# Optimization experiments

Measured on AMD Instinct MI355X. Metric: run time of the kernel, lower is better.

The kernel has to match this reference:

```python
import jax, jax.numpy as jnp
import numpy as np
import math

B, L, D = 2, 2048, 256
N_SETS, PLANES_PER_SET = 4, 4
TOTAL_PLANES = N_SETS * PLANES_PER_SET  # 16
POS_PLANES = 16
LTM_PLANES = POS_PLANES
PI = math.pi
LN_EPS = 1e-5


def _mlp2(x, w1, b1, w2, b2):
    h = jax.nn.gelu(x @ w1 + b1, approximate=False)  # torch nn.GELU default = erf
    return h @ w2 + b2


def setup_inputs() -> dict:
    key = jax.random.key(0)
    ks = iter(jax.random.split(key, 40))
    def W(shape):
        return jax.random.normal(next(ks), shape, jnp.float32) / np.float32(np.sqrt(shape[0]))
    z = lambda *s: jnp.zeros(s, jnp.float32)
    return dict(
        x=jax.random.normal(next(ks), (B, L, D), jnp.float32),
        ke_w1=W((D, D)), ke_b1=z(D), ke_w2=W((D, TOTAL_PLANES)), ke_b2=z(TOTAL_PLANES),
        qe_w1=W((D, D)), qe_b1=z(D), qe_w2=W((D, TOTAL_PLANES)), qe_b2=z(TOTAL_PLANES),
        v_w=W((D, D)), v_b=z(D),
        out_ln_g=jnp.ones(D, jnp.float32), out_ln_b=z(D),
        out_w=W((D, D)), out_b=z(D),
        set_weights=jnp.ones(N_SETS, jnp.float32),
        pos_weight=jnp.ones((), jnp.float32),
        gate_w1=W((D, D // 2)), gate_b1=z(D // 2), gate_w2=W((D // 2, 1)), gate_b2=z(1),
        lke_w1=W((D, D)), lke_b1=z(D), lke_w2=W((D, LTM_PLANES)), lke_b2=z(LTM_PLANES),
        surprise_scale=jnp.asarray(5.0, jnp.float32), surprise_bias=jnp.asarray(0.0, jnp.float32),
        resonance_scale=jnp.asarray(5.0, jnp.float32), resonance_threshold=jnp.asarray(0.3, jnp.float32),
        ltm_weight=jnp.asarray(0.5, jnp.float32),
        pos_freqs=jnp.exp(jnp.arange(POS_PLANES, dtype=jnp.float32) * (-math.log(10000.0) / POS_PLANES)),
        ltm_binding_mem=((jax.random.normal(next(ks), (LTM_PLANES, D))
                          + 1j * jax.random.normal(next(ks), (LTM_PLANES, D))) * 0.5).astype(jnp.complex64),
        ltm_count=jnp.asarray(100.0, jnp.float32),
    )


def reference(x, ke_w1, ke_b1, ke_w2, ke_b2, qe_w1, qe_b1, qe_w2, qe_b2,
              v_w, v_b, out_ln_g, out_ln_b, out_w, out_b,
              set_weights, pos_weight, gate_w1, gate_b1, gate_w2, gate_b2,
              lke_w1, lke_b1, lke_w2, lke_b2,
              surprise_scale, surprise_bias, resonance_scale, resonance_threshold,
              ltm_weight, pos_freqs, ltm_binding_mem, ltm_count):
    B_, L_, D_ = x.shape
    key_phasor = jnp.exp(1j * (jnp.tanh(_mlp2(x, ke_w1, ke_b1, ke_w2, ke_b2)) * PI))    # (B,L,16) complex64
    query_phasor = jnp.exp(1j * (jnp.tanh(_mlp2(x, qe_w1, qe_b1, qe_w2, qe_b2)) * PI))  # (B,L,16)
    kp = key_phasor.reshape(B_, L_, N_SETS, PLANES_PER_SET)
    qp = query_phasor.reshape(B_, L_, N_SETS, PLANES_PER_SET)
    weights = jax.nn.softmax(set_weights)
    V_real = x @ v_w + v_b                                                              # (B,L,D)

    # --- cross-bank surprise gate (n_sets > 1 branch) ---
    joint_key = jnp.prod(kp, axis=2)    # (B,L,PP)
    joint_query = jnp.prod(qp, axis=2)
    km = jnp.cumsum(joint_key, axis=1)
    key_memory = jnp.concatenate([jnp.zeros_like(km[:, :1]), km[:, :-1]], axis=1)       # shifted cumsum
    resonance_mag = jnp.abs(key_memory * jnp.conj(joint_query)).mean(-1, keepdims=True)
    positions = jnp.maximum(jnp.arange(L_, dtype=x.dtype), 1.0)
    norm_res = resonance_mag / jnp.sqrt(positions)[None, :, None]
    scale = jnp.clip(resonance_scale, 1.0, 20.0)
    thr = jnp.clip(resonance_threshold, 0.1, 0.9)
    surprise = 0.5 * (1.0 - jnp.tanh(scale * (norm_res - thr)))
    write_gate = jax.nn.sigmoid(surprise_scale * (surprise - 0.5) + surprise_bias)      # (B,L,1)
    Vg = (V_real * write_gate).astype(jnp.complex64)

    # --- cross-bank retrieval over joint (product) phasors ---
    bound = joint_key[..., None] * Vg[:, :, None, :]                                     # (B,L,PP,D)
    mem = jnp.cumsum(bound, axis=1)
    cross = jnp.real((mem * jnp.conj(joint_query)[..., None]).sum(2))                    # (B,L,D)

    # --- per-bank retrieval over all 16 planes ---
    bound_all = key_phasor[..., None] * Vg[:, :, None, :]                                # (B,L,16,D)
    mem_all = jnp.cumsum(bound_all, axis=1)
    ret_all = mem_all * jnp.conj(query_phasor)[..., None]
    per_bank = jnp.real(ret_all.reshape(B_, L_, N_SETS, PLANES_PER_SET, D_).sum(3))      # (B,L,S,D)
    total = (per_bank * weights[None, None, :, None]).sum(2)
    total = (total + cross) / (N_SETS + 1)

    # --- positional phase plane ---
    pos_phase = jnp.arange(L_, dtype=x.dtype)[:, None] * pos_freqs * (2.0 * PI)          # (L,16)
    pos_phasor = jnp.exp(1j * pos_phase)
    Vc = V_real.astype(jnp.complex64)
    bound_pos = pos_phasor[None, :, :, None] * Vc[:, :, None, :]                         # (B,L,16,D)
    mem_pos = jnp.cumsum(bound_pos, axis=1)
    ret_pos = jnp.real((mem_pos * jnp.conj(pos_phasor)[None, :, :, None]).sum(2))        # (B,L,D)
    gate = jax.nn.sigmoid(_mlp2(x, gate_w1, gate_b1, gate_w2, gate_b2))                  # (B,L,1)
    total = gate * total + (1.0 - gate) * (jax.nn.sigmoid(pos_weight) * ret_pos)

    # --- long-term memory retrieval (inference path; buffers are constants) ---
    ltm_phasor = jnp.exp(1j * (jnp.tanh(_mlp2(x, lke_w1, lke_b1, lke_w2, lke_b2)) * PI)) # (B,L,16)
    persistent = jnp.real((ltm_binding_mem[None, None] * jnp.conj(ltm_phasor)[..., None]).sum(2))
    pnorm = jnp.sqrt(jnp.maximum(ltm_count, 1.0) * LTM_PLANES)
    total = total + jax.nn.sigmoid(ltm_weight) * (persistent / pnorm)

    # --- to_out: LayerNorm + Linear ---
    mu = total.mean(-1, keepdims=True)
    var = ((total - mu) ** 2).mean(-1, keepdims=True)
    h = (total - mu) / jnp.sqrt(var + LN_EPS) * out_ln_g + out_ln_b
    return h @ out_w + out_b
```

## Files before the change

kernel.cpp:

```cpp
#include <hip/hip_runtime.h>
#include <hip/hip_bf16.h>
#include <math.h>

#define BB 2
#define LL 2048
#define DD 256
#define NT (BB*LL)
#define HCOLS 896
#define NCOLS 1152
#define KBIG 768
#define FDIM 80
#define CC 64
#define NC (NT/CC)
#define NCB (LL/CC)
#define SST (FDIM*DD)
#define PI_F 3.14159265358979323846f

typedef __attribute__((ext_vector_type(8))) short s8frag;
typedef __attribute__((ext_vector_type(4))) float f4acc;

#define GLDS16(g, l) __builtin_amdgcn_global_load_lds( \
    (const __attribute__((address_space(1))) void*)(g), \
    (__attribute__((address_space(3))) void*)(l), 16, 0, 0)

__device__ __forceinline__ float gelu_erf(float v) {
    return 0.5f * v * (1.0f + erff(v * 0.70710678118654752440f));
}
__device__ __forceinline__ float sigmoidf_(float v) {
    return 1.0f / (1.0f + expf(-v));
}
__device__ __forceinline__ unsigned short bf16bits(__hip_bfloat16 h) {
    return *reinterpret_cast<unsigned short*>(&h);
}

#define K0A_BLKS (NT * DD / 4 / 256)
#define K0B_TW   22
#define K0B_BLKS ((KBIG / 64) * K0B_TW)
#define K0C_BLKS (4 * 16 * 768 / 256)
#define K0D_BLKS 5
__global__ __launch_bounds__(256) void k0_prep(
    const float* __restrict__ x,
    const float* __restrict__ ke_w1, const float* __restrict__ ke_b1,
    const float* __restrict__ qe_w1, const float* __restrict__ qe_b1,
    const float* __restrict__ lke_w1, const float* __restrict__ lke_b1,
    const float* __restrict__ gate_w1, const float* __restrict__ gate_b1,
    const float* __restrict__ v_w, const float* __restrict__ v_b,
    const float* __restrict__ ke_w2, const float* __restrict__ qe_w2,
    const float* __restrict__ lke_w2, const float* __restrict__ gate_w2,
    const float* __restrict__ out_w,
    __hip_bfloat16* __restrict__ xhi, __hip_bfloat16* __restrict__ xlo,
    __hip_bfloat16* __restrict__ BT, float* __restrict__ bcat,
    __hip_bfloat16* __restrict__ W2T, __hip_bfloat16* __restrict__ OWT)
{
    __shared__ float tile[64][65];
    const int b = blockIdx.x, tid = threadIdx.x;
    if (b < K0A_BLKS) {
        int idx = b * 256 + tid;
        float4 v = reinterpret_cast<const float4*>(x)[idx];
        float vv[4] = {v.x, v.y, v.z, v.w};
        #pragma unroll
        for (int j = 0; j < 4; ++j) {
            __hip_bfloat16 h = __float2bfloat16(vv[j]);
            xhi[idx * 4 + j] = h;
            xlo[idx * 4 + j] = __float2bfloat16(vv[j] - __bfloat162float(h));
        }
    } else if (b < K0A_BLKS + K0B_BLKS) {
        int bb = b - K0A_BLKS;
        int bk = bb / K0B_TW, bn = bb - bk * K0B_TW;
        int kp0 = bk * 64, n0 = bn * 64;
        int seg = kp0 >> 8;
        int k0 = kp0 - seg * 256;
        #pragma unroll 4
        for (int i = 0; i < 16; ++i) {
            int kl = i * 4 + (tid >> 6);
            int nl = tid & 63;
            int k = k0 + kl, n = n0 + nl;
            float w;
            if (n < 256)       w = ke_w1[k * 256 + n];
            else if (n < 512)  w = qe_w1[k * 256 + (n - 256)];
            else if (n < 768)  w = lke_w1[k * 256 + (n - 512)];
            else if (n < 896)  w = gate_w1[k * 128 + (n - 768)];
            else if (n < 1152) w = v_w[k * 256 + (n - 896)];
            else               w = out_w[k * 256 + (n - 1152)];
            tile[kl][nl] = w;
        }
        __syncthreads();
        #pragma unroll 4
        for (int i = 0; i < 16; ++i) {
            int nl = i * 4 + (tid >> 6);
            int kpl = tid & 63;
            float w = tile[kpl][nl];
            __hip_bfloat16 hi = __float2bfloat16(w);
            __hip_bfloat16 out = (seg == 1)
                ? __float2bfloat16(w - __bfloat162float(hi)) : hi;
            if (n0 < 1152)
                BT[(size_t)(n0 + nl) * KBIG + kp0 + kpl] = out;
            else
                OWT[(size_t)(n0 + nl - 1152) * KBIG + kp0 + kpl] = out;
        }
    } else if (b < K0A_BLKS + K0B_BLKS + K0C_BLKS) {
        int idx = (b - K0A_BLKS - K0B_BLKS) * 256 + tid;
        int g = idx / (16 * 768);
        int rem = idx - g * (16 * 768);
        int n = rem / 768;
        int kp = rem - n * 768;
        float w = 0.0f;
        int seg;
        if (g < 3) {
            seg = kp >> 8;
            int k = kp & 255;
            const float* W = (g == 0) ? ke_w2 : (g == 1) ? qe_w2 : lke_w2;
            w = W[k * 16 + n];
        } else {
            seg = kp >> 7;
            int k = kp & 127;
            if (n == 0 && kp < 384) w = gate_w2[k];
            else { seg = 0; w = 0.0f; }
        }
        __hip_bfloat16 hi = __float2bfloat16(w);
        __hip_bfloat16 out = (seg == 1) ? __float2bfloat16(w - __bfloat162float(hi)) : hi;
        W2T[idx] = out;
    } else {
        int n = (b - K0A_BLKS - K0B_BLKS - K0C_BLKS) * 256 + tid;
        if (n < NCOLS) {
            float bia;
            if (n < 256)      bia = ke_b1[n];
            else if (n < 512) bia = qe_b1[n - 256];
            else if (n < 768) bia = lke_b1[n - 512];
            else if (n < 896) bia = gate_b1[n - 768];
            else              bia = v_b[n - 896];
            bcat[n] = bia;
        }
    }
}

__global__ __launch_bounds__(256) void k1_mfma(
    const __hip_bfloat16* __restrict__ xhi, const __hip_bfloat16* __restrict__ xlo,
    const __hip_bfloat16* __restrict__ BT, const float* __restrict__ bcat,
    __hip_bfloat16* __restrict__ Hhi, __hip_bfloat16* __restrict__ Hlo,
    float* __restrict__ V)
{
    __shared__ __align__(16) short As[128 * 64];
    __shared__ __align__(16) short Bs[64 * 64];
    const int tid = threadIdx.x;
    const int wave = tid >> 6, lane = tid & 63;
    const int wr = wave >> 1, wc = wave & 1;
    const int bm = blockIdx.x, bn = blockIdx.y;
    const int lg = lane >> 4, lr = lane & 15;

    f4acc acc[4][2] = {};

    for (int kt = 0; kt < KBIG / 64; ++kt) {
        const int k0 = kt * 64;
        const __hip_bfloat16* xsrc = (kt < 8) ? xhi : xlo;
        const int kcol = (kt < 8) ? (k0 & 255) : (k0 - 512);
        #pragma unroll
        for (int j = 0; j < 4; ++j) {
            int r0 = wave * 32 + j * 8;
            int row = r0 + (lane >> 3);
            int ch = (lane & 7) ^ (row & 7);
            GLDS16(xsrc + (size_t)(bm * 128 + row) * DD + kcol + ch * 8, &As[r0 * 64]);
        }
        #pragma unroll
        for (int j = 0; j < 2; ++j) {
            int r0 = wave * 16 + j * 8;
            int row = r0 + (lane >> 3);
            int ch = (lane & 7) ^ (row & 7);
            GLDS16(BT + (size_t)(bn * 64 + row) * KBIG + k0 + ch * 8, &Bs[r0 * 64]);
        }
        __syncthreads();
        #pragma unroll
        for (int kk = 0; kk < 2; ++kk) {
            s8frag a[4], b[2];
            #pragma unroll
            for (int i = 0; i < 4; ++i) {
                int arow = wr * 64 + i * 16 + lr;
                int slot = (kk * 4 + lg) ^ (arow & 7);
                a[i] = *reinterpret_cast<const s8frag*>(&As[arow * 64 + slot * 8]);
            }
            #pragma unroll
            for (int i = 0; i < 2; ++i) {
                int brow = wc * 32 + i * 16 + lr;
                int slot = (kk * 4 + lg) ^ (brow & 7);
                b[i] = *reinterpret_cast<const s8frag*>(&Bs[brow * 64 + slot * 8]);
            }
            #pragma unroll
            for (int mi = 0; mi < 4; ++mi)
                #pragma unroll
                for (int ni = 0; ni < 2; ++ni)
                    acc[mi][ni] = __builtin_amdgcn_mfma_f32_16x16x32_bf16(
                        a[mi], b[ni], acc[mi][ni], 0, 0, 0);
        }
        __syncthreads();
    }

    #pragma unroll
    for (int ni = 0; ni < 2; ++ni) {
        int n = bn * 64 + wc * 32 + ni * 16 + lr;
        float bia = bcat[n];
        #pragma unroll
        for (int mi = 0; mi < 4; ++mi) {
            #pragma unroll
            for (int r = 0; r < 4; ++r) {
                int m = bm * 128 + wr * 64 + mi * 16 + lg * 4 + r;
                float v = acc[mi][ni][r] + bia;
                if (n < HCOLS) {
                    float hv = gelu_erf(v);
                    __hip_bfloat16 h = __float2bfloat16(hv);
                    Hhi[(size_t)m * HCOLS + n] = h;
                    Hlo[(size_t)m * HCOLS + n] = __float2bfloat16(hv - __bfloat162float(h));
                } else {
                    V[(size_t)m * DD + (n - HCOLS)] = v;
                }
            }
        }
    }
}

__global__ __launch_bounds__(256) void k2_fused(
    const __hip_bfloat16* __restrict__ Hhi, const __hip_bfloat16* __restrict__ Hlo,
    const __hip_bfloat16* __restrict__ W2T,
    const float* __restrict__ ke_b2, const float* __restrict__ qe_b2,
    const float* __restrict__ lke_b2, const float* __restrict__ gate_b2,
    const float* __restrict__ set_weights, const float* __restrict__ pos_weight,
    const float* __restrict__ ltm_weight, const float* __restrict__ ltm_count,
    const float* __restrict__ pos_freqs,
    float* __restrict__ Fk, float* __restrict__ Fq, float* __restrict__ Fql,
    float* __restrict__ J)
{
    __shared__ float c2s[32][52];
    const int tid = threadIdx.x;
    const int g = tid >> 6, lane = tid & 63;
    const int lg = lane >> 4, lr = lane & 15;
    const int t0 = blockIdx.x * 32;

    {
        const int seglen = (g < 3) ? 256 : 128;
        const int gbase = (g < 3) ? g * 256 : 768;
        const int nsteps = (g < 3) ? 24 : 12;
        const __hip_bfloat16* wbase = W2T + (size_t)(g * 16 + lr) * 768;
        f4acc acc[2] = {};
        for (int kt = 0; kt < nsteps; ++kt) {
            const int kp = kt * 32;
            const int seg = kp / seglen;
            const int kk = kp - seg * seglen;
            const __hip_bfloat16* asrc = (seg < 2) ? Hhi : Hlo;
            const int col = gbase + kk + lg * 8;
            s8frag b = *reinterpret_cast<const s8frag*>(wbase + kp + lg * 8);
            #pragma unroll
            for (int mi = 0; mi < 2; ++mi) {
                s8frag a = *reinterpret_cast<const s8frag*>(
                    asrc + (size_t)(t0 + mi * 16 + lr) * HCOLS + col);
                acc[mi] = __builtin_amdgcn_mfma_f32_16x16x32_bf16(a, b, acc[mi], 0, 0, 0);
            }
        }
        int col = g * 16 + lr;
        if (col < 49) {
            #pragma unroll
            for (int mi = 0; mi < 2; ++mi)
                #pragma unroll
                for (int r = 0; r < 4; ++r)
                    c2s[mi * 16 + lg * 4 + r][col] = acc[mi][r];
        }
    }
    __syncthreads();

    for (int i = tid; i < 32 * 64; i += 256) {
        int t = i >> 6, c = i & 63;
        if (c < 49) {
            float a = c2s[t][c];
            float val;
            if (c < 16)      val = tanhf(a + ke_b2[c]) * PI_F;
            else if (c < 32) val = tanhf(a + qe_b2[c - 16]) * PI_F;
            else if (c < 48) val = tanhf(a + lke_b2[c - 32]) * PI_F;
            else             val = sigmoidf_(a + gate_b2[0]);
            c2s[t][c] = val;
        }
    }
    __syncthreads();

    float sw[4];
    {
        float s0 = set_weights[0], s1 = set_weights[1], s2 = set_weights[2], s3 = set_weights[3];
        float mx = fmaxf(fmaxf(s0, s1), fmaxf(s2, s3));
        float e0 = expf(s0 - mx), e1 = expf(s1 - mx), e2 = expf(s2 - mx), e3 = expf(s3 - mx);
        float inv = 1.0f / (e0 + e1 + e2 + e3);
        sw[0] = e0 * inv; sw[1] = e1 * inv; sw[2] = e2 * inv; sw[3] = e3 * inv;
    }
    const float spw = sigmoidf_(pos_weight[0]);
    const float altm = sigmoidf_(ltm_weight[0]) / sqrtf(fmaxf(ltm_count[0], 1.0f) * 16.0f);
    const int sg = tid >> 5, sl = tid & 31;

    for (int tr = 0; tr < 4; ++tr) {
        const int lt = tr * 8 + sg;
        const int t = t0 + lt;
        const float gg = c2s[lt][48];
        const float aq = gg * 0.2f;
        const float apos = (1.0f - gg) * spw;
        const int l = t & (LL - 1);
        float* fkr  = Fk  + (size_t)t * FDIM;
        float* fqr  = Fq  + (size_t)t * FDIM;
        float* fqlr = Fql + (size_t)t * 32;

        if (sl < 16) {
            int p = sl;
            float sk, ck; sincosf(c2s[lt][p], &sk, &ck);
            fkr[2 * p] = ck; fkr[2 * p + 1] = sk;
            float sq, cq; sincosf(c2s[lt][16 + p], &sq, &cq);
            float wq = aq * sw[p >> 2];
            fqr[2 * p] = wq * cq; fqr[2 * p + 1] = wq * sq;
            float sl_, cl_; sincosf(c2s[lt][32 + p], &sl_, &cl_);
            fqlr[2 * p] = altm * cl_; fqlr[2 * p + 1] = altm * sl_;
            float th = (float)l * pos_freqs[p] * (2.0f * PI_F);
            float sp, cp; sincosf(th, &sp, &cp);
            fkr[40 + 2 * p] = cp; fkr[41 + 2 * p] = sp;
            fqr[40 + 2 * p] = apos * cp; fqr[41 + 2 * p] = apos * sp;
        } else if (sl < 20) {
            int p = sl - 16;
            float pjk = c2s[lt][p] + c2s[lt][p + 4] + c2s[lt][p + 8] + c2s[lt][p + 12];
            float pjq = c2s[lt][16 + p] + c2s[lt][20 + p] + c2s[lt][24 + p] + c2s[lt][28 + p];
            float sjk, cjk; sincosf(pjk, &sjk, &cjk);
            float sjq, cjq; sincosf(pjq, &sjq, &cjq);
            fkr[32 + 2 * p] = cjk; fkr[33 + 2 * p] = sjk;
            fqr[32 + 2 * p] = aq * cjq; fqr[33 + 2 * p] = aq * sjq;
            J[(size_t)(2 * p) * NT + t] = cjk;
            J[(size_t)(2 * p + 1) * NT + t] = sjk;
        } else if (sl < 24) {
            int p = sl - 20;
            fkr[72 + 2 * p] = 0.0f; fkr[73 + 2 * p] = 0.0f;
            fqr[72 + 2 * p] = 0.0f; fqr[73 + 2 * p] = 0.0f;
        }
    }
}

__device__ __forceinline__ int swz2048(int l) {
    return (l & ~31) | ((l ^ (l >> 5)) & 31);
}
__global__ __launch_bounds__(512) void k3a_scan(
    const float* __restrict__ J, float* __restrict__ wg,
    const float* __restrict__ resonance_scale, const float* __restrict__ resonance_threshold,
    const float* __restrict__ surprise_scale, const float* __restrict__ surprise_bias)
{
    __shared__ float km[8 * LL];
    const int b = blockIdx.x;
    const int tid = threadIdx.x;
    const int w = tid >> 6;
    const int lane = tid & 63;
    {
        float v[32];
        float s = 0.0f;
        int l0 = lane * 32;
        const float4* src = reinterpret_cast<const float4*>(
            J + (size_t)w * NT + b * LL + l0);
        #pragma unroll
        for (int i = 0; i < 8; ++i) {
            float4 q = src[i];
            v[4 * i + 0] = q.x; v[4 * i + 1] = q.y;
            v[4 * i + 2] = q.z; v[4 * i + 3] = q.w;
            s += q.x + q.y + q.z + q.w;
        }
        float local = s;
        #pragma unroll
        for (int off = 1; off < 64; off <<= 1) {
            float n = __shfl_up(s, off);
            if (lane >= off) s += n;
        }
        float run = s - local;
        #pragma unroll 4
        for (int i = 0; i < 32; ++i) { km[w * LL + swz2048(l0 + i)] = run; run += v[i]; }
    }
    __syncthreads();
    const float sc  = fminf(fmaxf(resonance_scale[0], 1.0f), 20.0f);
    const float th  = fminf(fmaxf(resonance_threshold[0], 0.1f), 0.9f);
    const float ssc = surprise_scale[0];
    const float sbi = surprise_bias[0];
    for (int q = 0; q < 4; ++q) {
        int l = tid + 512 * q;
        int ls = swz2048(l);
        float rm = 0.0f;
        #pragma unroll
        for (int p = 0; p < 4; ++p) {
            float re = km[(2 * p) * LL + ls], im = km[(2 * p + 1) * LL + ls];
            rm += sqrtf(re * re + im * im);
        }
        rm *= 0.25f;
        float nr = rm / sqrtf(fmaxf((float)l, 1.0f));
        float sur = 0.5f * (1.0f - tanhf(sc * (nr - th)));
        wg[b * LL + l] = sigmoidf_(ssc * (sur - 0.5f) + sbi);
    }
}

__global__ __launch_bounds__(256) void k4a_state(
    const float* __restrict__ Fk, const float* __restrict__ wg,
    const float* __restrict__ V, float* __restrict__ S)
{
    __shared__ __align__(16) float fk[CC][FDIM];
    const int c = blockIdx.x;
    const int f0 = blockIdx.y * 20;
    const int tid = threadIdx.x;
    for (int i = tid; i < CC * FDIM; i += 256) {
        int r = i / FDIM, cx = i - r * FDIM;
        float f = Fk[(size_t)c * CC * FDIM + i];
        if (cx < 40) f *= wg[c * CC + r];
        fk[r][cx] = f;
    }
    __syncthreads();
    float acc[20];
    #pragma unroll
    for (int f = 0; f < 20; ++f) acc[f] = 0.0f;
    const float* vp = V + (size_t)c * CC * DD + tid;
    for (int r = 0; r < CC; ++r) {
        float v = vp[(size_t)r * DD];
        #pragma unroll
        for (int g = 0; g < 5; ++g) {
            float4 q = *reinterpret_cast<const float4*>(&fk[r][f0 + 4 * g]);
            acc[4 * g + 0] += q.x * v; acc[4 * g + 1] += q.y * v;
            acc[4 * g + 2] += q.z * v; acc[4 * g + 3] += q.w * v;
        }
    }
    float* sp = S + (size_t)c * SST + tid;
    #pragma unroll
    for (int f = 0; f < 20; ++f) sp[(size_t)(f0 + f) * DD] = acc[f];
}

__global__ __launch_bounds__(256) void k4b_scan(
    const float* __restrict__ S, float* __restrict__ M)
{
    const int e = blockIdx.x * 256 + threadIdx.x;
    const int b = blockIdx.y;
    float run = 0.0f;
    #pragma unroll 8
    for (int cc = 0; cc < NCB; ++cc) {
        size_t o = ((size_t)(b * NCB + cc)) * SST + e;
        M[o] = run;
        run += S[o];
    }
}

__global__ __launch_bounds__(256) void k4c_out(
    const float* __restrict__ Fq, const float* __restrict__ Fk,
    const float* __restrict__ wg, const float* __restrict__ Fql,
    const float* __restrict__ V, const float* __restrict__ M,
    const float* __restrict__ ltm_mem, float* __restrict__ Tot)
{
    __shared__ __align__(16) float fq[16][FDIM];
    __shared__ __align__(16) float fkS[CC * 96];
    __shared__ __align__(16) float sc[16][68];
    const int c = blockIdx.x;
    const int h = blockIdx.y;
    const int r0 = h * 16;
    const int nrows = r0 + 16;
    const int tid = threadIdx.x;

    for (int i = tid; i < 16 * FDIM; i += 256) {
        int r = i / FDIM, cx = i - r * FDIM;
        fq[r][cx] = Fq[(size_t)(c * CC + r0 + r) * FDIM + cx];
    }
    for (int i = tid; i < nrows * FDIM; i += 256) {
        int r = i / FDIM, cx = i - r * FDIM;
        float f = Fk[(size_t)c * CC * FDIM + i];
        if (cx < 40) f *= wg[c * CC + r];
        fkS[r * 96 + (cx ^ ((r & 7) << 2))] = f;
    }
    __syncthreads();

    #pragma unroll
    for (int q = 0; q < 4; ++q) {
        int idx = tid + 256 * q;
        int i = idx >> 6, j = idx & 63;
        float s = 0.0f;
        if (r0 + i >= j) {
            const int sw = (j & 7) << 2;
            #pragma unroll
            for (int g = 0; g < 20; ++g) {
                float4 a = *reinterpret_cast<const float4*>(&fq[i][4 * g]);
                float4 b = *reinterpret_cast<const float4*>(&fkS[j * 96 + ((4 * g) ^ sw)]);
                s += a.x * b.x + a.y * b.y + a.z * b.z + a.w * b.w;
            }
        }
        sc[i][j] = s;
    }
    __syncthreads();

    const int d = tid;
    float acc[16];
    #pragma unroll
    for (int i = 0; i < 16; ++i) acc[i] = 0.0f;

    const float* mp = M + (size_t)c * SST + d;
    #pragma unroll 2
    for (int g = 0; g < 20; ++g) {
        float m0 = mp[(size_t)(4 * g + 0) * DD];
        float m1 = mp[(size_t)(4 * g + 1) * DD];
        float m2 = mp[(size_t)(4 * g + 2) * DD];
        float m3 = mp[(size_t)(4 * g + 3) * DD];
        #pragma unroll
        for (int i = 0; i < 16; ++i) {
            float4 a = *reinterpret_cast<const float4*>(&fq[i][4 * g]);
            acc[i] += a.x * m0 + a.y * m1 + a.z * m2 + a.w * m3;
        }
    }
    const float* vp = V + (size_t)c * CC * DD + d;
    const int j4max = nrows >> 2;
    #pragma unroll 2
    for (int j4 = 0; j4 < j4max; ++j4) {
        float v0 = vp[(size_t)(4 * j4 + 0) * DD];
        float v1 = vp[(size_t)(4 * j4 + 1) * DD];
        float v2 = vp[(size_t)(4 * j4 + 2) * DD];
        float v3 = vp[(size_t)(4 * j4 + 3) * DD];
        #pragma unroll
        for (int i = 0; i < 16; ++i) {
            float4 s4 = *reinterpret_cast<const float4*>(&sc[i][4 * j4]);
            acc[i] += s4.x * v0 + s4.y * v1 + s4.z * v2 + s4.w * v3;
        }
    }
    float mre[16], mim[16];
    #pragma unroll
    for (int p = 0; p < 16; ++p) {
        mre[p] = ltm_mem[((size_t)p * DD + d) * 2];
        mim[p] = ltm_mem[((size_t)p * DD + d) * 2 + 1];
    }
    __syncthreads();
    for (int i = tid; i < 16 * 32; i += 256) {
        int r = i >> 5, p = i & 31;
        sc[r][p] = Fql[(size_t)(c * CC + r0 + r) * 32 + p];
    }
    __syncthreads();
    float* tp = Tot + (size_t)(c * CC + r0) * DD + d;
    #pragma unroll 1
    for (int i = 0; i < 16; ++i) {
        float a = acc[i];
        #pragma unroll
        for (int p = 0; p < 16; ++p)
            a += sc[i][2 * p] * mre[p] + sc[i][2 * p + 1] * mim[p];
        tp[(size_t)i * DD] = a;
    }
}

__global__ __launch_bounds__(256) void k5a_ln(
    const float* __restrict__ Tot,
    const float* __restrict__ gln, const float* __restrict__ bln,
    __hip_bfloat16* __restrict__ Hnhi, __hip_bfloat16* __restrict__ Hnlo)
{
    const int tid = threadIdx.x;
    const int t0 = blockIdx.x * 16;
    const int w = tid >> 6, lane = tid & 63;
    const int r = 4 * w + (lane >> 4);
    const int l4 = lane & 15;
    const int t = t0 + r;
    float vbuf[16];
    float s = 0.0f, s2 = 0.0f;
    const float4* src = reinterpret_cast<const float4*>(
        Tot + (size_t)t * DD + l4 * 16);
    #pragma unroll
    for (int g = 0; g < 4; ++g) {
        float4 v = src[g];
        vbuf[4 * g + 0] = v.x; vbuf[4 * g + 1] = v.y;
        vbuf[4 * g + 2] = v.z; vbuf[4 * g + 3] = v.w;
        s += v.x + v.y + v.z + v.w;
        s2 += v.x * v.x + v.y * v.y + v.z * v.z + v.w * v.w;
    }
    #pragma unroll
    for (int off = 1; off < 16; off <<= 1) {
        s  += __shfl_xor(s, off);
        s2 += __shfl_xor(s2, off);
    }
    float mu = s * (1.0f / 256.0f);
    float var = s2 * (1.0f / 256.0f) - mu * mu;
    float rstd = rsqrtf(var + 1e-5f);
    unsigned hw[8], lw[8];
    #pragma unroll
    for (int j = 0; j < 8; ++j) {
        unsigned short h0, h1, l0, l1;
        #pragma unroll
        for (int e = 0; e < 2; ++e) {
            int i = 2 * j + e;
            int k = l4 * 16 + i;
            float hn = (vbuf[i] - mu) * rstd * gln[k] + bln[k];
            __hip_bfloat16 hb = __float2bfloat16(hn);
            __hip_bfloat16 lb = __float2bfloat16(hn - __bfloat162float(hb));
            if (e == 0) { h0 = bf16bits(hb); l0 = bf16bits(lb); }
            else        { h1 = bf16bits(hb); l1 = bf16bits(lb); }
        }
        hw[j] = (unsigned)h0 | ((unsigned)h1 << 16);
        lw[j] = (unsigned)l0 | ((unsigned)l1 << 16);
    }
    uint4* dh = reinterpret_cast<uint4*>(Hnhi + (size_t)t * DD + l4 * 16);
    uint4* dl = reinterpret_cast<uint4*>(Hnlo + (size_t)t * DD + l4 * 16);
    dh[0] = make_uint4(hw[0], hw[1], hw[2], hw[3]);
    dh[1] = make_uint4(hw[4], hw[5], hw[6], hw[7]);
    dl[0] = make_uint4(lw[0], lw[1], lw[2], lw[3]);
    dl[1] = make_uint4(lw[4], lw[5], lw[6], lw[7]);
}

__global__ __launch_bounds__(256) void k5b_mfma(
    const __hip_bfloat16* __restrict__ Hnhi, const __hip_bfloat16* __restrict__ Hnlo,
    const __hip_bfloat16* __restrict__ OWT, const float* __restrict__ out_b,
    float* __restrict__ out)
{
    __shared__ __align__(16) short As[64 * 64];
    __shared__ __align__(16) short Bs[64 * 64];
    const int tid = threadIdx.x;
    const int wave = tid >> 6, lane = tid & 63;
    const int wr = wave >> 1, wc = wave & 1;
    const int bm = blockIdx.x, bn = blockIdx.y;
    const int lg = lane >> 4, lr = lane & 15;

    f4acc acc[2][2] = {};

    for (int kt = 0; kt < KBIG / 64; ++kt) {
        const int k0 = kt * 64;
        const __hip_bfloat16* asrc = (kt < 8) ? Hnhi : Hnlo;
        const int kcol = (kt < 8) ? (k0 & 255) : (k0 - 512);
        #pragma unroll
        for (int j = 0; j < 2; ++j) {
            int r0 = wave * 16 + j * 8;
            int row = r0 + (lane >> 3);
            int ch = (lane & 7) ^ (row & 7);
            GLDS16(asrc + (size_t)(bm * 64 + row) * DD + kcol + ch * 8, &As[r0 * 64]);
            GLDS16(OWT + (size_t)(bn * 64 + row) * KBIG + k0 + ch * 8, &Bs[r0 * 64]);
        }
        __syncthreads();
        #pragma unroll
        for (int kk = 0; kk < 2; ++kk) {
            s8frag a[2], b[2];
            #pragma unroll
            for (int i = 0; i < 2; ++i) {
                int arow = wr * 32 + i * 16 + lr;
                int aslot = (kk * 4 + lg) ^ (arow & 7);
                a[i] = *reinterpret_cast<const s8frag*>(&As[arow * 64 + aslot * 8]);
                int brow = wc * 32 + i * 16 + lr;
                int bslot = (kk * 4 + lg) ^ (brow & 7);
                b[i] = *reinterpret_cast<const s8frag*>(&Bs[brow * 64 + bslot * 8]);
            }
            #pragma unroll
            for (int mi = 0; mi < 2; ++mi)
                #pragma unroll
                for (int ni = 0; ni < 2; ++ni)
                    acc[mi][ni] = __builtin_amdgcn_mfma_f32_16x16x32_bf16(
                        a[mi], b[ni], acc[mi][ni], 0, 0, 0);
        }
        __syncthreads();
    }

    #pragma unroll
    for (int ni = 0; ni < 2; ++ni) {
        int n = bn * 64 + wc * 32 + ni * 16 + lr;
        float ob = out_b[n];
        #pragma unroll
        for (int mi = 0; mi < 2; ++mi) {
            #pragma unroll
            for (int r = 0; r < 4; ++r) {
                int m = bm * 64 + wr * 32 + mi * 16 + lg * 4 + r;
                out[(size_t)m * DD + n] = acc[mi][ni][r] + ob;
            }
        }
    }
}

extern "C" void kernel_launch(void* const* d_in, const int* in_sizes, int n_in,
                              void* d_out, int out_size, void* d_ws, size_t ws_size,
                              hipStream_t stream)
{
    (void)in_sizes; (void)n_in; (void)out_size; (void)ws_size;
    const float* x        = (const float*)d_in[0];
    const float* ke_w1    = (const float*)d_in[1];
    const float* ke_b1    = (const float*)d_in[2];
    const float* ke_w2    = (const float*)d_in[3];
    const float* ke_b2    = (const float*)d_in[4];
    const float* qe_w1    = (const float*)d_in[5];
    const float* qe_b1    = (const float*)d_in[6];
    const float* qe_w2    = (const float*)d_in[7];
    const float* qe_b2    = (const float*)d_in[8];
    const float* v_w      = (const float*)d_in[9];
    const float* v_b      = (const float*)d_in[10];
    const float* out_ln_g = (const float*)d_in[11];
    const float* out_ln_b = (const float*)d_in[12];
    const float* out_w    = (const float*)d_in[13];
    const float* out_b    = (const float*)d_in[14];
    const float* set_weights = (const float*)d_in[15];
    const float* pos_weight  = (const float*)d_in[16];
    const float* gate_w1  = (const float*)d_in[17];
    const float* gate_b1  = (const float*)d_in[18];
    const float* gate_w2  = (const float*)d_in[19];
    const float* gate_b2  = (const float*)d_in[20];
    const float* lke_w1   = (const float*)d_in[21];
    const float* lke_b1   = (const float*)d_in[22];
    const float* lke_w2   = (const float*)d_in[23];
    const float* lke_b2   = (const float*)d_in[24];
    const float* surprise_scale      = (const float*)d_in[25];
    const float* surprise_bias       = (const float*)d_in[26];
    const float* resonance_scale     = (const float*)d_in[27];
    const float* resonance_threshold = (const float*)d_in[28];
    const float* ltm_weight = (const float*)d_in[29];
    const float* pos_freqs  = (const float*)d_in[30];
    const float* ltm_mem    = (const float*)d_in[31];
    const float* ltm_count  = (const float*)d_in[32];

    float* ws  = (float*)d_ws;
    float* Hf  = ws;
    float* V   = Hf  + (size_t)NT * HCOLS;
    float* Fk  = V   + (size_t)NT * DD;
    float* Fq  = Fk  + (size_t)NT * FDIM;
    float* Fql = Fq  + (size_t)NT * FDIM;
    float* Tot = Fql + (size_t)NT * 32;
    float* J   = Tot + (size_t)NT * DD;
    __hip_bfloat16* W2T = (__hip_bfloat16*)(J + (size_t)NT * 8);
    float* wg  = (float*)(W2T + 4 * 16 * 768);
    __hip_bfloat16* OWT = (__hip_bfloat16*)(wg + NT);

    __hip_bfloat16* Hhi = (__hip_bfloat16*)Hf;
    __hip_bfloat16* Hlo = Hhi + (size_t)NT * HCOLS;
    float* S   = Hf;
    float* M   = Hf + (size_t)NC * SST;
    __hip_bfloat16* Hnhi = (__hip_bfloat16*)Hf;
    __hip_bfloat16* Hnlo = Hnhi + (size_t)NT * DD;
    __hip_bfloat16* xhi = (__hip_bfloat16*)Fk;
    __hip_bfloat16* xlo = xhi + (size_t)NT * DD;
    __hip_bfloat16* BT  = xlo + (size_t)NT * DD;
    float* bcat = (float*)(BT + (size_t)NCOLS * KBIG);

    k0_prep<<<K0A_BLKS + K0B_BLKS + K0C_BLKS + K0D_BLKS, 256, 0, stream>>>(
        x, ke_w1, ke_b1, qe_w1, qe_b1, lke_w1, lke_b1, gate_w1, gate_b1, v_w, v_b,
        ke_w2, qe_w2, lke_w2, gate_w2, out_w, xhi, xlo, BT, bcat, W2T, OWT);
    k1_mfma<<<dim3(NT / 128, NCOLS / 64), 256, 0, stream>>>(xhi, xlo, BT, bcat,
                                                            Hhi, Hlo, V);
    k2_fused<<<NT / 32, 256, 0, stream>>>(Hhi, Hlo, W2T,
                                          ke_b2, qe_b2, lke_b2, gate_b2,
                                          set_weights, pos_weight,
                                          ltm_weight, ltm_count, pos_freqs,
                                          Fk, Fq, Fql, J);
    k3a_scan<<<BB, 512, 0, stream>>>(J, wg, resonance_scale, resonance_threshold,
                                     surprise_scale, surprise_bias);
    k4a_state<<<dim3(NC, 4), 256, 0, stream>>>(Fk, wg, V, S);
    k4b_scan<<<dim3(SST / 256, BB), 256, 0, stream>>>(S, M);
    k4c_out<<<dim3(NC, 4), 256, 0, stream>>>(Fq, Fk, wg, Fql, V, M, ltm_mem, Tot);
    k5a_ln<<<NT / 16, 256, 0, stream>>>(Tot, out_ln_g, out_ln_b, Hnhi, Hnlo);
    k5b_mfma<<<dim3(NT / 64, DD / 64), 256, 0, stream>>>(Hnhi, Hnlo, OWT, out_b,
                                                         (float*)d_out);
}
```

Measured before the change: 123.6 us.

## Double-buffer k1 GEMM LDS staging and fuse LayerNorm into k4c output kernel

The k1 MFMA GEMM now keeps two LDS buffers and issues the global-to-LDS loads for the next K tile before computing on the current one, so loads can overlap the MFMAs. Separately, the LayerNorm (and its bf16 hi/lo split) moves into the k4c output kernel: each block reduces row sums with wave shuffles plus shared memory, then writes the normalized bf16 pairs directly. This removes the Tot round trip through global memory and one kernel launch. The cost is twice the LDS in k1, which may lower occupancy, and extra syncs and reductions in k4c.

```diff
diff --git a/kernel.cpp b/kernel.cpp
--- a/kernel.cpp
+++ b/kernel.cpp
@@ -140,8 +140,8 @@
     __hip_bfloat16* __restrict__ Hhi, __hip_bfloat16* __restrict__ Hlo,
     float* __restrict__ V)
 {
-    __shared__ __align__(16) short As[128 * 64];
-    __shared__ __align__(16) short Bs[64 * 64];
+    __shared__ __align__(16) short As[2][128 * 64];
+    __shared__ __align__(16) short Bs[2][64 * 64];
     const int tid = threadIdx.x;
     const int wave = tid >> 6, lane = tid & 63;
     const int wr = wave >> 1, wc = wave & 1;
@@ -150,7 +150,7 @@
 
     f4acc acc[4][2] = {};
 
-    for (int kt = 0; kt < KBIG / 64; ++kt) {
+    auto stage = [&](int buf, int kt) {
         const int k0 = kt * 64;
         const __hip_bfloat16* xsrc = (kt < 8) ? xhi : xlo;
         const int kcol = (kt < 8) ? (k0 & 255) : (k0 - 512);
@@ -159,16 +159,24 @@
             int r0 = wave * 32 + j * 8;
             int row = r0 + (lane >> 3);
             int ch = (lane & 7) ^ (row & 7);
-            GLDS16(xsrc + (size_t)(bm * 128 + row) * DD + kcol + ch * 8, &As[r0 * 64]);
+            GLDS16(xsrc + (size_t)(bm * 128 + row) * DD + kcol + ch * 8,
+                   &As[buf][r0 * 64]);
         }
         #pragma unroll
         for (int j = 0; j < 2; ++j) {
             int r0 = wave * 16 + j * 8;
             int row = r0 + (lane >> 3);
             int ch = (lane & 7) ^ (row & 7);
-            GLDS16(BT + (size_t)(bn * 64 + row) * KBIG + k0 + ch * 8, &Bs[r0 * 64]);
-        }
-        __syncthreads();
+            GLDS16(BT + (size_t)(bn * 64 + row) * KBIG + k0 + ch * 8,
+                   &Bs[buf][r0 * 64]);
+        }
+    };
+
+    stage(0, 0);
+    __syncthreads();
+    int cur = 0;
+    for (int kt = 0; kt < KBIG / 64; ++kt) {
+        if (kt + 1 < KBIG / 64) stage(cur ^ 1, kt + 1);
         #pragma unroll
         for (int kk = 0; kk < 2; ++kk) {
             s8frag a[4], b[2];
@@ -176,13 +184,13 @@
             for (int i = 0; i < 4; ++i) {
                 int arow = wr * 64 + i * 16 + lr;
                 int slot = (kk * 4 + lg) ^ (arow & 7);
-                a[i] = *reinterpret_cast<const s8frag*>(&As[arow * 64 + slot * 8]);
+                a[i] = *reinterpret_cast<const s8frag*>(&As[cur][arow * 64 + slot * 8]);
             }
             #pragma unroll
             for (int i = 0; i < 2; ++i) {
                 int brow = wc * 32 + i * 16 + lr;
                 int slot = (kk * 4 + lg) ^ (brow & 7);
-                b[i] = *reinterpret_cast<const s8frag*>(&Bs[brow * 64 + slot * 8]);
+                b[i] = *reinterpret_cast<const s8frag*>(&Bs[cur][brow * 64 + slot * 8]);
             }
             #pragma unroll
             for (int mi = 0; mi < 4; ++mi)
@@ -192,6 +200,7 @@
                         a[mi], b[ni], acc[mi][ni], 0, 0, 0);
         }
         __syncthreads();
+        cur ^= 1;
     }
 
     #pragma unroll
@@ -437,11 +446,13 @@
     }
 }
 
-__global__ __launch_bounds__(256) void k4c_out(
+__global__ __launch_bounds__(256) void k4c_ln(
     const float* __restrict__ Fq, const float* __restrict__ Fk,
     const float* __restrict__ wg, const float* __restrict__ Fql,
     const float* __restrict__ V, const float* __restrict__ M,
-    const float* __restrict__ ltm_mem, float* __restrict__ Tot)
+    const float* __restrict__ ltm_mem,
+    const float* __restrict__ gln, const float* __restrict__ bln,
+    __hip_bfloat16* __restrict__ Hnhi, __hip_bfloat16* __restrict__ Hnlo)
 {
     __shared__ __align__(16) float fq[16][FDIM];
     __shared__ __align__(16) float fkS[CC * 96];
@@ -451,6 +462,7 @@
     const int r0 = h * 16;
     const int nrows = r0 + 16;
     const int tid = threadIdx.x;
+    const int wave = tid >> 6, lane = tid & 63;
 
     for (int i = tid; i < 16 * FDIM; i += 256) {
         int r = i / FDIM, cx = i - r * FDIM;
@@ -526,71 +538,42 @@
         sc[r][p] = Fql[(size_t)(c * CC + r0 + r) * 32 + p];
     }
     __syncthreads();
-    float* tp = Tot + (size_t)(c * CC + r0) * DD + d;
     #pragma unroll 1
     for (int i = 0; i < 16; ++i) {
         float a = acc[i];
         #pragma unroll
         for (int p = 0; p < 16; ++p)
             a += sc[i][2 * p] * mre[p] + sc[i][2 * p + 1] * mim[p];
-        tp[(size_t)i * DD] = a;
-    }
-}
-
-__global__ __launch_bounds__(256) void k5a_ln(
-    const float* __restrict__ Tot,
-    const float* __restrict__ gln, const float* __restrict__ bln,
-    __hip_bfloat16* __restrict__ Hnhi, __hip_bfloat16* __restrict__ Hnlo)
-{
-    const int tid = threadIdx.x;
-    const int t0 = blockIdx.x * 16;
-    const int w = tid >> 6, lane = tid & 63;
-    const int r = 4 * w + (lane >> 4);
-    const int l4 = lane & 15;
-    const int t = t0 + r;
-    float vbuf[16];
-    float s = 0.0f, s2 = 0.0f;
-    const float4* src = reinterpret_cast<const float4*>(
-        Tot + (size_t)t * DD + l4 * 16);
+        acc[i] = a;
+    }
+    __syncthreads();
+
     #pragma unroll
-    for (int g = 0; g < 4; ++g) {
-        float4 v = src[g];
-        vbuf[4 * g + 0] = v.x; vbuf[4 * g + 1] = v.y;
-        vbuf[4 * g + 2] = v.z; vbuf[4 * g + 3] = v.w;
-        s += v.x + v.y + v.z + v.w;
-        s2 += v.x * v.x + v.y * v.y + v.z * v.z + v.w * v.w;
-    }
-    #pragma unroll
-    for (int off = 1; off < 16; off <<= 1) {
-        s  += __shfl_xor(s, off);
-        s2 += __shfl_xor(s2, off);
-    }
-    float mu = s * (1.0f / 256.0f);
-    float var = s2 * (1.0f / 256.0f) - mu * mu;
-    float rstd = rsqrtf(var + 1e-5f);
-    unsigned hw[8], lw[8];
-    #pragma unroll
-    for (int j = 0; j < 8; ++j) {
-        unsigned short h0, h1, l0, l1;
-        #pragma unroll
-        for (int e = 0; e < 2; ++e) {
-            int i = 2 * j + e;
-            int k = l4 * 16 + i;
-            float hn = (vbuf[i] - mu) * rstd * gln[k] + bln[k];
-            __hip_bfloat16 hb = __float2bfloat16(hn);
-            __hip_bfloat16 lb = __float2bfloat16(hn - __bfloat162float(hb));
-            if (e == 0) { h0 = bf16bits(hb); l0 = bf16bits(lb); }
-            else        { h1 = bf16bits(hb); l1 = bf16bits(lb); }
-        }
-        hw[j] = (unsigned)h0 | ((unsigned)h1 << 16);
-        lw[j] = (unsigned)l0 | ((unsigned)l1 << 16);
-    }
-    uint4* dh = reinterpret_cast<uint4*>(Hnhi + (size_t)t * DD + l4 * 16);
-    uint4* dl = reinterpret_cast<uint4*>(Hnlo + (size_t)t * DD + l4 * 16);
-    dh[0] = make_uint4(hw[0], hw[1], hw[2], hw[3]);
-    dh[1] = make_uint4(hw[4], hw[5], hw[6], hw[7]);
-    dl[0] = make_uint4(lw[0], lw[1], lw[2], lw[3]);
-    dl[1] = make_uint4(lw[4], lw[5], lw[6], lw[7]);
+    for (int i = 0; i < 16; ++i) {
+        float s = acc[i], s2 = acc[i] * acc[i];
+        #pragma unroll
+        for (int off = 1; off < 64; off <<= 1) {
+            s  += __shfl_xor(s, off);
+            s2 += __shfl_xor(s2, off);
+        }
+        if (lane == 0) { sc[i][wave] = s; sc[i][4 + wave] = s2; }
+    }
+    __syncthreads();
+    const float gv = gln[d], bv = bln[d];
+    __hip_bfloat16* hp = Hnhi + (size_t)(c * CC + r0) * DD + d;
+    __hip_bfloat16* lp = Hnlo + (size_t)(c * CC + r0) * DD + d;
+    #pragma unroll 1
+    for (int i = 0; i < 16; ++i) {
+        float s  = sc[i][0] + sc[i][1] + sc[i][2] + sc[i][3];
+        float s2 = sc[i][4] + sc[i][5] + sc[i][6] + sc[i][7];
+        float mu = s * (1.0f / 256.0f);
+        float var = s2 * (1.0f / 256.0f) - mu * mu;
+        float rstd = rsqrtf(var + 1e-5f);
+        float hn = (acc[i] - mu) * rstd * gv + bv;
+        __hip_bfloat16 hb = __float2bfloat16(hn);
+        hp[(size_t)i * DD] = hb;
+        lp[(size_t)i * DD] = __float2bfloat16(hn - __bfloat162float(hb));
+    }
 }
 
 __global__ __launch_bounds__(256) void k5b_mfma(
@@ -734,8 +717,8 @@
                                      surprise_scale, surprise_bias);
     k4a_state<<<dim3(NC, 4), 256, 0, stream>>>(Fk, wg, V, S);
     k4b_scan<<<dim3(SST / 256, BB), 256, 0, stream>>>(S, M);
-    k4c_out<<<dim3(NC, 4), 256, 0, stream>>>(Fq, Fk, wg, Fql, V, M, ltm_mem, Tot);
-    k5a_ln<<<NT / 16, 256, 0, stream>>>(Tot, out_ln_g, out_ln_b, Hnhi, Hnlo);
+    k4c_ln<<<dim3(NC, 4), 256, 0, stream>>>(Fq, Fk, wg, Fql, V, M, ltm_mem,
+                                            out_ln_g, out_ln_b, Hnhi, Hnlo);
     k5b_mfma<<<dim3(NT / 64, DD / 64), 256, 0, stream>>>(Hnhi, Hnlo, OWT, out_b,
                                                          (float*)d_out);
 }
```

After: 127.1 us. +2.8%, slower.
